# Kernel tuning notes

Measured on AMD Instinct MI355X. Metric: run time of the kernel, lower is better.

The kernel has to match this reference:

```python
import jax, jax.numpy as jnp
import numpy as np

N_ELEC = 64
IN_C = 64
HID = [64, 128]
OUT_C = 128
BATCH = 2048
BN_EPS = 1e-5


def build_graph():
    """Replicates EEGGraphNet._build_graph_structure with random 3D electrode positions."""
    rng = np.random.RandomState(0)
    pos = rng.rand(N_ELEC, 3).astype(np.float64)
    d = np.sqrt(((pos[:, None, :] - pos[None, :, :]) ** 2).sum(-1))
    thr = np.percentile(d[d > 0], 30)
    src, dst = [], []
    for i in range(N_ELEC):
        for j in range(i + 1, N_ELEC):
            if d[i, j] < thr:
                src += [i, j]
                dst += [j, i]
    return np.asarray(src, np.int32), np.asarray(dst, np.int32)


def setup_inputs() -> dict:
    key = jax.random.key(0)
    ks = jax.random.split(key, 8)
    src, dst = build_graph()
    dims = [IN_C] + HID + [OUT_C]  # [64, 64, 128, 128]
    inp = {"x": jax.random.normal(ks[0], (BATCH, N_ELEC, IN_C), jnp.float32)}
    for li in range(3):
        fi, fo = dims[li], dims[li + 1]
        inp[f"W{li+1}"] = jax.random.normal(ks[li + 1], (fi, fo), jnp.float32) * (1.0 / np.sqrt(fi))
        inp[f"b{li+1}"] = jnp.zeros((fo,), jnp.float32)
    for li in range(2):  # BN after first two convs
        inp[f"g{li+1}"] = jnp.ones((dims[li + 1],), jnp.float32)
        inp[f"be{li+1}"] = jnp.zeros((dims[li + 1],), jnp.float32)
    inp["src"] = jnp.asarray(src)
    inp["dst"] = jnp.asarray(dst)
    return inp


def gcn_conv(x, W, b, src, dst, edge_norm, self_norm):
    # x: (B, N, Fin) -> (B, N, Fout). GCN with self-loops, symmetric norm.
    h = jnp.einsum("bnf,fo->bno", x, W)
    msg = h[:, src, :] * edge_norm[None, :, None]          # (B, E, Fout) gather
    agg = jnp.zeros_like(h).at[:, dst, :].add(msg)         # scatter-add over dst
    return agg + h * self_norm[None, :, None] + b


def batchnorm(x, g, be):
    # torch BatchNorm1d over flattened (B*N, C) nodes, training-mode batch stats
    m = jnp.mean(x, axis=(0, 1))
    v = jnp.mean((x - m) ** 2, axis=(0, 1))
    return g * (x - m) * jax.lax.rsqrt(v + BN_EPS) + be


def reference(x, W1, b1, W2, b2, W3, b3, g1, be1, g2, be2, src, dst):
    # degree (with self-loop) is identical across graphs in the batch
    deg = jnp.zeros((N_ELEC,), x.dtype).at[dst].add(1.0) + 1.0
    inv_sqrt = jax.lax.rsqrt(deg)
    edge_norm = inv_sqrt[src] * inv_sqrt[dst]
    self_norm = 1.0 / deg

    h = gcn_conv(x, W1, b1, src, dst, edge_norm, self_norm)
    h = jax.nn.relu(batchnorm(h, g1, be1))
    h = gcn_conv(h, W2, b2, src, dst, edge_norm, self_norm)
    h = jax.nn.relu(batchnorm(h, g2, be2))
    h = gcn_conv(h, W3, b3, src, dst, edge_norm, self_norm)
    return jnp.mean(h, axis=1)  # global mean pool over electrodes -> (B, OUT_C)
```

## Files before the change

kernel.cpp:

```cpp
#include <hip/hip_runtime.h>
#include <hip/hip_bf16.h>

typedef unsigned short ushortT;
typedef unsigned int uintT;
typedef __attribute__((ext_vector_type(8))) short short8;
typedef __attribute__((ext_vector_type(4))) float f32x4;

#define BATCH   2048
#define NELEC   64
#define BN_EPS  1e-5f

#define OFF_AMEAN  4096
#define OFF_SS1    4160
#define OFF_SS2    4288
#define OFF_PS1    4544
#define OFF_PQ1    8640
#define OFF_PS2    12736
#define OFF_PQ2    20928
#define OFF_ABF    29120
#define OFF_W1T    33216
#define OFF_W2T    37312
#define OFF_H1     45504
#define OFF_H2     4239808

#define MFMA(a, b, c) __builtin_amdgcn_mfma_f32_16x16x32_bf16(a, b, c, 0, 0, 0)

__device__ inline float bf2f(ushortT u) { return __uint_as_float(((uintT)u) << 16); }
__device__ inline ushortT f2bf(float f) {
  uintT u = __float_as_uint(f);
  u = (u + 0x7FFFu + ((u >> 16) & 1u)) >> 16;
  return (ushortT)u;
}
__device__ inline void split2(float f, ushortT& hi, ushortT& lo) {
  hi = f2bf(f);
  lo = f2bf(f - bf2f(hi));
}
__device__ inline void split8(const float* f, short8& hi, short8& lo) {
  #pragma unroll
  for (int e = 0; e < 8; ++e) {
    ushortT h, l;
    split2(f[e], h, l);
    hi[e] = (short)h; lo[e] = (short)l;
  }
}

__global__ __launch_bounds__(256) void prep_kernel(const int* __restrict__ src,
    const int* __restrict__ dst, int E,
    const float* __restrict__ W1, const float* __restrict__ W2,
    float* __restrict__ ws) {
  __shared__ float degS[NELEC];
  __shared__ float As[NELEC * NELEC];
  int t = threadIdx.x;
  if (t < NELEC) degS[t] = 1.0f;
  for (int i = t; i < NELEC * NELEC; i += 256) As[i] = 0.0f;
  __syncthreads();
  for (int e = t; e < E; e += 256) atomicAdd(&degS[dst[e]], 1.0f);
  __syncthreads();
  for (int e = t; e < E; e += 256) {
    float en = rsqrtf(degS[src[e]]) * rsqrtf(degS[dst[e]]);
    atomicAdd(&As[dst[e] * NELEC + src[e]], en);
  }
  __syncthreads();
  if (t < NELEC) As[t * NELEC + t] += 1.0f / degS[t];
  __syncthreads();
  ushortT* abf = (ushortT*)(ws + OFF_ABF);
  for (int i = t; i < 4096; i += 256) {
    ushortT hi, lo; split2(As[i], hi, lo);
    abf[i] = hi; abf[4096 + i] = lo;
  }
  if (t < NELEC) {
    float s = 0.0f;
    for (int n = 0; n < NELEC; ++n) s += As[n * NELEC + t];
    ws[OFF_AMEAN + t] = s * (1.0f / NELEC);
  }
  ushortT* w1t = (ushortT*)(ws + OFF_W1T);
  for (int i = t; i < 4096; i += 256) {
    int o = i >> 6, k = i & 63;
    ushortT hi, lo; split2(W1[k * 64 + o], hi, lo);
    w1t[i] = hi; w1t[4096 + i] = lo;
  }
  ushortT* w2t = (ushortT*)(ws + OFF_W2T);
  for (int i = t; i < 8192; i += 256) {
    int o = i >> 6, k = i & 63;
    ushortT hi, lo; split2(W2[k * 128 + o], hi, lo);
    w2t[i] = hi; w2t[8192 + i] = lo;
  }
}

__global__ __launch_bounds__(256) void layer1_mfma(const float* __restrict__ x,
    const float* __restrict__ b1, float* __restrict__ ws) {
  __shared__ ushortT TsH[4][16 * 72];
  __shared__ ushortT TsL[4][16 * 72];
  const int w = threadIdx.x >> 6, lane = threadIdx.x & 63;
  const int item = blockIdx.x * 4 + w;
  const int c = lane & 15, g = lane >> 4;
  const ushortT* abf = (const ushortT*)(ws + OFF_ABF);
  const ushortT* w1t = (const ushortT*)(ws + OFF_W1T);
  ushortT* h1p = (ushortT*)(ws + OFF_H1) + (size_t)item * 4096;
  ushortT* tsh = &TsH[w][0];
  ushortT* tsl = &TsL[w][0];

  short8 Xhi[4][2], Xlo[4][2];
  #pragma unroll
  for (int rt = 0; rt < 4; ++rt) {
    #pragma unroll
    for (int ks = 0; ks < 2; ++ks) {
      const float* p = x + (size_t)item * 4096 + (rt * 16 + c) * 64 + ks * 32 + g * 8;
      float4 fa = *(const float4*)p;
      float4 fb = *(const float4*)(p + 4);
      float f[8] = {fa.x, fa.y, fa.z, fa.w, fb.x, fb.y, fb.z, fb.w};
      split8(f, Xhi[rt][ks], Xlo[rt][ks]);
    }
  }

  for (int s = 0; s < 4; ++s) {
    f32x4 t[4] = {{0,0,0,0},{0,0,0,0},{0,0,0,0},{0,0,0,0}};
    #pragma unroll
    for (int ks = 0; ks < 2; ++ks) {
      short8 bh = *(const short8*)(w1t + (s * 16 + c) * 64 + ks * 32 + g * 8);
      short8 bl = *(const short8*)(w1t + 4096 + (s * 16 + c) * 64 + ks * 32 + g * 8);
      #pragma unroll
      for (int rt = 0; rt < 4; ++rt) {
        t[rt] = MFMA(Xhi[rt][ks], bh, t[rt]);
        t[rt] = MFMA(Xhi[rt][ks], bl, t[rt]);
        t[rt] = MFMA(Xlo[rt][ks], bh, t[rt]);
      }
    }
    #pragma unroll
    for (int rt = 0; rt < 4; ++rt) {
      ushortT h0, h1_, h2_, h3, l0, l1, l2, l3;
      split2(t[rt][0], h0, l0); split2(t[rt][1], h1_, l1);
      split2(t[rt][2], h2_, l2); split2(t[rt][3], h3, l3);
      uint2 wh, wl;
      wh.x = (uintT)h0 | ((uintT)h1_ << 16); wh.y = (uintT)h2_ | ((uintT)h3 << 16);
      wl.x = (uintT)l0 | ((uintT)l1 << 16);  wl.y = (uintT)l2 | ((uintT)l3 << 16);
      int idx = c * 72 + rt * 16 + g * 4;
      *(uint2*)(tsh + idx) = wh;
      *(uint2*)(tsl + idx) = wl;
    }
    f32x4 hacc[4] = {{0,0,0,0},{0,0,0,0},{0,0,0,0},{0,0,0,0}};
    #pragma unroll
    for (int ks = 0; ks < 2; ++ks) {
      short8 th = *(const short8*)(tsh + c * 72 + ks * 32 + g * 8);
      short8 tl = *(const short8*)(tsl + c * 72 + ks * 32 + g * 8);
      #pragma unroll
      for (int rt = 0; rt < 4; ++rt) {
        short8 ah = *(const short8*)(abf + (rt * 16 + c) * 64 + ks * 32 + g * 8);
        short8 al = *(const short8*)(abf + 4096 + (rt * 16 + c) * 64 + ks * 32 + g * 8);
        hacc[rt] = MFMA(ah, th, hacc[rt]);
        hacc[rt] = MFMA(ah, tl, hacc[rt]);
        hacc[rt] = MFMA(al, th, hacc[rt]);
      }
    }
    float bias = b1[s * 16 + c];
    float S = 0.0f, Q = 0.0f;
    #pragma unroll
    for (int rt = 0; rt < 4; ++rt) {
      #pragma unroll
      for (int r = 0; r < 4; ++r) {
        float v = hacc[rt][r] + bias;
        S += v; Q += v * v;
        h1p[(rt * 16 + g * 4 + r) * 64 + s * 16 + c] = f2bf(v);
      }
    }
    S += __shfl_xor(S, 16); S += __shfl_xor(S, 32);
    Q += __shfl_xor(Q, 16); Q += __shfl_xor(Q, 32);
    if (g == 0) {
      int slot = item & 63;
      atomicAdd(&ws[OFF_PS1 + slot * 64 + s * 16 + c], S);
      atomicAdd(&ws[OFF_PQ1 + slot * 64 + s * 16 + c], Q);
    }
  }
}

__global__ void reduce1_kernel(const float* __restrict__ g1, const float* __restrict__ be1,
                               float* __restrict__ ws) {
  int t = threadIdx.x;
  if (t < 64) {
    float S = 0.0f, Q = 0.0f;
    for (int s = 0; s < 64; ++s) { S += ws[OFF_PS1 + s * 64 + t]; Q += ws[OFF_PQ1 + s * 64 + t]; }
    const float inv = 1.0f / (float)(BATCH * NELEC);
    float m = S * inv;
    float v = fmaxf(Q * inv - m * m, 0.0f);
    float sc = g1[t] * rsqrtf(v + BN_EPS);
    ws[OFF_SS1 + t] = sc;
    ws[OFF_SS1 + 64 + t] = fmaf(-m, sc, be1[t]);
  }
}

__global__ void reduce2_kernel(const float* __restrict__ g2, const float* __restrict__ be2,
                               float* __restrict__ ws) {
  int t = threadIdx.x;
  if (t < 128) {
    float S = 0.0f, Q = 0.0f;
    for (int s = 0; s < 64; ++s) { S += ws[OFF_PS2 + s * 128 + t]; Q += ws[OFF_PQ2 + s * 128 + t]; }
    const float inv = 1.0f / (float)(BATCH * NELEC);
    float m = S * inv;
    float v = fmaxf(Q * inv - m * m, 0.0f);
    float sc = g2[t] * rsqrtf(v + BN_EPS);
    ws[OFF_SS2 + t] = sc;
    ws[OFF_SS2 + 128 + t] = fmaf(-m, sc, be2[t]);
  }
}

__global__ __launch_bounds__(256) void layer2_mfma(const float* __restrict__ b2,
    float* __restrict__ ws) {
  __shared__ ushortT TsH[4][16 * 72];
  __shared__ ushortT TsL[4][16 * 72];
  const int w = threadIdx.x >> 6, lane = threadIdx.x & 63;
  const int item = blockIdx.x * 4 + w;
  const int c = lane & 15, g = lane >> 4;
  const ushortT* abf = (const ushortT*)(ws + OFF_ABF);
  const ushortT* w2t = (const ushortT*)(ws + OFF_W2T);
  const ushortT* h1p = (const ushortT*)(ws + OFF_H1) + (size_t)item * 4096;
  ushortT* h2p = (ushortT*)(ws + OFF_H2) + (size_t)item * 8192;
  ushortT* tsh = &TsH[w][0];
  ushortT* tsl = &TsL[w][0];

  short8 Yhi[4][2], Ylo[4][2];
  #pragma unroll
  for (int ks = 0; ks < 2; ++ks) {
    const float* sp = ws + OFF_SS1 + ks * 32 + g * 8;
    const float* tp = ws + OFF_SS1 + 64 + ks * 32 + g * 8;
    float4 sa = *(const float4*)sp, sb = *(const float4*)(sp + 4);
    float4 ta = *(const float4*)tp, tb = *(const float4*)(tp + 4);
    float s8[8] = {sa.x, sa.y, sa.z, sa.w, sb.x, sb.y, sb.z, sb.w};
    float t8[8] = {ta.x, ta.y, ta.z, ta.w, tb.x, tb.y, tb.z, tb.w};
    #pragma unroll
    for (int rt = 0; rt < 4; ++rt) {
      short8 hv = *(const short8*)(h1p + (rt * 16 + c) * 64 + ks * 32 + g * 8);
      float f[8];
      #pragma unroll
      for (int e = 0; e < 8; ++e)
        f[e] = fmaxf(fmaf(bf2f((ushortT)hv[e]), s8[e], t8[e]), 0.0f);
      split8(f, Yhi[rt][ks], Ylo[rt][ks]);
    }
  }

  for (int s = 0; s < 8; ++s) {
    f32x4 t[4] = {{0,0,0,0},{0,0,0,0},{0,0,0,0},{0,0,0,0}};
    #pragma unroll
    for (int ks = 0; ks < 2; ++ks) {
      short8 bh = *(const short8*)(w2t + (s * 16 + c) * 64 + ks * 32 + g * 8);
      short8 bl = *(const short8*)(w2t + 8192 + (s * 16 + c) * 64 + ks * 32 + g * 8);
      #pragma unroll
      for (int rt = 0; rt < 4; ++rt) {
        t[rt] = MFMA(Yhi[rt][ks], bh, t[rt]);
        t[rt] = MFMA(Yhi[rt][ks], bl, t[rt]);
        t[rt] = MFMA(Ylo[rt][ks], bh, t[rt]);
      }
    }
    #pragma unroll
    for (int rt = 0; rt < 4; ++rt) {
      ushortT h0, h1_, h2_, h3, l0, l1, l2, l3;
      split2(t[rt][0], h0, l0); split2(t[rt][1], h1_, l1);
      split2(t[rt][2], h2_, l2); split2(t[rt][3], h3, l3);
      uint2 wh, wl;
      wh.x = (uintT)h0 | ((uintT)h1_ << 16); wh.y = (uintT)h2_ | ((uintT)h3 << 16);
      wl.x = (uintT)l0 | ((uintT)l1 << 16);  wl.y = (uintT)l2 | ((uintT)l3 << 16);
      int idx = c * 72 + rt * 16 + g * 4;
      *(uint2*)(tsh + idx) = wh;
      *(uint2*)(tsl + idx) = wl;
    }
    f32x4 hacc[4] = {{0,0,0,0},{0,0,0,0},{0,0,0,0},{0,0,0,0}};
    #pragma unroll
    for (int ks = 0; ks < 2; ++ks) {
      short8 th = *(const short8*)(tsh + c * 72 + ks * 32 + g * 8);
      short8 tl = *(const short8*)(tsl + c * 72 + ks * 32 + g * 8);
      #pragma unroll
      for (int rt = 0; rt < 4; ++rt) {
        short8 ah = *(const short8*)(abf + (rt * 16 + c) * 64 + ks * 32 + g * 8);
        short8 al = *(const short8*)(abf + 4096 + (rt * 16 + c) * 64 + ks * 32 + g * 8);
        hacc[rt] = MFMA(ah, th, hacc[rt]);
        hacc[rt] = MFMA(ah, tl, hacc[rt]);
        hacc[rt] = MFMA(al, th, hacc[rt]);
      }
    }
    float bias = b2[s * 16 + c];
    float S = 0.0f, Q = 0.0f;
    #pragma unroll
    for (int rt = 0; rt < 4; ++rt) {
      #pragma unroll
      for (int r = 0; r < 4; ++r) {
        float v = hacc[rt][r] + bias;
        S += v; Q += v * v;
        h2p[(rt * 16 + g * 4 + r) * 128 + s * 16 + c] = f2bf(v);
      }
    }
    S += __shfl_xor(S, 16); S += __shfl_xor(S, 32);
    Q += __shfl_xor(Q, 16); Q += __shfl_xor(Q, 32);
    if (g == 0) {
      int slot = item & 63;
      atomicAdd(&ws[OFF_PS2 + slot * 128 + s * 16 + c], S);
      atomicAdd(&ws[OFF_PQ2 + slot * 128 + s * 16 + c], Q);
    }
  }
}

__global__ __launch_bounds__(256) void layer3_kernel(const float* __restrict__ W3,
    const float* __restrict__ b3, const float* __restrict__ ws,
    float* __restrict__ out) {
  const int w = threadIdx.x >> 6, lane = threadIdx.x & 63;
  const int item = blockIdx.x * 4 + w;
  const int f0 = lane * 2;
  const float s2a = ws[OFF_SS2 + f0],       s2b = ws[OFF_SS2 + f0 + 1];
  const float t2a = ws[OFF_SS2 + 128 + f0], t2b = ws[OFF_SS2 + 128 + f0 + 1];
  const float* am = ws + OFF_AMEAN;
  const ushortT* h2 = (const ushortT*)(ws + OFF_H2) + (size_t)item * 8192;
  float v0 = 0.0f, v1 = 0.0f;
  #pragma unroll 8
  for (int m = 0; m < 64; ++m) {
    uintT pk = *(const uintT*)(h2 + m * 128 + f0);
    float y0 = fmaxf(fmaf(bf2f((ushortT)(pk & 0xffffu)), s2a, t2a), 0.0f);
    float y1 = fmaxf(fmaf(bf2f((ushortT)(pk >> 16)),     s2b, t2b), 0.0f);
    float a = am[m];
    v0 = fmaf(a, y0, v0);
    v1 = fmaf(a, y1, v1);
  }
  float o0 = b3[f0], o1 = b3[f0 + 1];
  #pragma unroll 8
  for (int k = 0; k < 128; ++k) {
    float vk = __shfl((k & 1) ? v1 : v0, k >> 1, 64);
    o0 = fmaf(vk, W3[k * 128 + f0],     o0);
    o1 = fmaf(vk, W3[k * 128 + f0 + 1], o1);
  }
  float2 ov; ov.x = o0; ov.y = o1;
  *(float2*)(out + (size_t)item * 128 + f0) = ov;
}

extern "C" void kernel_launch(void* const* d_in, const int* in_sizes, int n_in,
                              void* d_out, int out_size, void* d_ws, size_t ws_size,
                              hipStream_t stream) {
  const float* x   = (const float*)d_in[0];
  const float* W1  = (const float*)d_in[1];
  const float* b1  = (const float*)d_in[2];
  const float* W2  = (const float*)d_in[3];
  const float* b2  = (const float*)d_in[4];
  const float* W3  = (const float*)d_in[5];
  const float* b3  = (const float*)d_in[6];
  const float* g1  = (const float*)d_in[7];
  const float* be1 = (const float*)d_in[8];
  const float* g2  = (const float*)d_in[9];
  const float* be2 = (const float*)d_in[10];
  const int*   src = (const int*)d_in[11];
  const int*   dst = (const int*)d_in[12];
  const int E = in_sizes[11];
  float* ws  = (float*)d_ws;
  float* out = (float*)d_out;

  hipMemsetAsync((void*)(ws + OFF_PS1), 0, (size_t)(29120 - OFF_PS1) * 4, stream);
  hipLaunchKernelGGL(prep_kernel,   dim3(1),   dim3(256), 0, stream, src, dst, E, W1, W2, ws);
  hipLaunchKernelGGL(layer1_mfma,   dim3(512), dim3(256), 0, stream, x, b1, ws);
  hipLaunchKernelGGL(reduce1_kernel,dim3(1),   dim3(64),  0, stream, g1, be1, ws);
  hipLaunchKernelGGL(layer2_mfma,   dim3(512), dim3(256), 0, stream, b2, ws);
  hipLaunchKernelGGL(reduce2_kernel,dim3(1),   dim3(128), 0, stream, g2, be2, ws);
  hipLaunchKernelGGL(layer3_kernel, dim3(512), dim3(256), 0, stream, W3, b3, ws, out);
}
```

Baseline: 200.9 us.

## Process one graph per block, split output column tiles across waves

Each layer kernel now gives one batch item to a whole 256-thread block, and the four waves split the output feature tiles instead of each wave looping over all tiles. Inputs are loaded coalesced into shared memory, split into hi/lo bf16 there and shared by all waves. Intermediate activations are stored tile-major (16-column blocks) so the per-wave writes are contiguous, and layer 3 reads with the matching layout. This raises parallelism and shortens the serial per-wave loop, at the cost of a block barrier and more shared memory per block.

```diff
diff --git a/kernel.cpp b/kernel.cpp
--- a/kernel.cpp
+++ b/kernel.cpp
@@ -87,89 +87,100 @@
   }
 }
 
-__global__ __launch_bounds__(256) void layer1_mfma(const float* __restrict__ x,
+__global__ __launch_bounds__(256, 4) void layer1_mfma(const float* __restrict__ x,
     const float* __restrict__ b1, float* __restrict__ ws) {
-  __shared__ ushortT TsH[4][16 * 72];
-  __shared__ ushortT TsL[4][16 * 72];
-  const int w = threadIdx.x >> 6, lane = threadIdx.x & 63;
-  const int item = blockIdx.x * 4 + w;
-  const int c = lane & 15, g = lane >> 4;
+  __shared__ ushortT FH[4096];
+  __shared__ ushortT FL[4096];
+  __shared__ ushortT Ts[4][2][1152];
+  const int item = blockIdx.x, t = threadIdx.x;
+  {
+    const int m = t >> 2, q = t & 3;
+    const float* xp = x + (size_t)item * 4096 + m * 64 + q * 16;
+    float f[16];
+    *(float4*)&f[0]  = *(const float4*)(xp);
+    *(float4*)&f[4]  = *(const float4*)(xp + 4);
+    *(float4*)&f[8]  = *(const float4*)(xp + 8);
+    *(float4*)&f[12] = *(const float4*)(xp + 12);
+    short8 h0, l0, h1v, l1v;
+    split8(f, h0, l0);
+    split8(f + 8, h1v, l1v);
+    const int base = q * 1024 + m * 8;
+    *(short8*)&FH[base] = h0; *(short8*)&FH[base + 512] = h1v;
+    *(short8*)&FL[base] = l0; *(short8*)&FL[base + 512] = l1v;
+  }
+  __syncthreads();
+  const int w = t >> 6, lane = t & 63, c = lane & 15, g = lane >> 4;
+  short8 Xhi[4][2], Xlo[4][2];
+  #pragma unroll
+  for (int rt = 0; rt < 4; ++rt) {
+    #pragma unroll
+    for (int ks = 0; ks < 2; ++ks) {
+      const int a = (ks * 4 + g) * 512 + (rt * 16 + c) * 8;
+      Xhi[rt][ks] = *(const short8*)&FH[a];
+      Xlo[rt][ks] = *(const short8*)&FL[a];
+    }
+  }
   const ushortT* abf = (const ushortT*)(ws + OFF_ABF);
   const ushortT* w1t = (const ushortT*)(ws + OFF_W1T);
-  ushortT* h1p = (ushortT*)(ws + OFF_H1) + (size_t)item * 4096;
-  ushortT* tsh = &TsH[w][0];
-  ushortT* tsl = &TsL[w][0];
-
-  short8 Xhi[4][2], Xlo[4][2];
+  ushortT* tsh = &Ts[w][0][0];
+  ushortT* tsl = &Ts[w][1][0];
+  const int s = w;
+  f32x4 tacc[4] = {{0,0,0,0},{0,0,0,0},{0,0,0,0},{0,0,0,0}};
+  #pragma unroll
+  for (int ks = 0; ks < 2; ++ks) {
+    short8 bh = *(const short8*)(w1t + (s * 16 + c) * 64 + ks * 32 + g * 8);
+    short8 bl = *(const short8*)(w1t + 4096 + (s * 16 + c) * 64 + ks * 32 + g * 8);
+    #pragma unroll
+    for (int rt = 0; rt < 4; ++rt) {
+      tacc[rt] = MFMA(Xhi[rt][ks], bh, tacc[rt]);
+      tacc[rt] = MFMA(Xhi[rt][ks], bl, tacc[rt]);
+      tacc[rt] = MFMA(Xlo[rt][ks], bh, tacc[rt]);
+    }
+  }
   #pragma unroll
   for (int rt = 0; rt < 4; ++rt) {
-    #pragma unroll
-    for (int ks = 0; ks < 2; ++ks) {
-      const float* p = x + (size_t)item * 4096 + (rt * 16 + c) * 64 + ks * 32 + g * 8;
-      float4 fa = *(const float4*)p;
-      float4 fb = *(const float4*)(p + 4);
-      float f[8] = {fa.x, fa.y, fa.z, fa.w, fb.x, fb.y, fb.z, fb.w};
-      split8(f, Xhi[rt][ks], Xlo[rt][ks]);
-    }
-  }
-
-  for (int s = 0; s < 4; ++s) {
-    f32x4 t[4] = {{0,0,0,0},{0,0,0,0},{0,0,0,0},{0,0,0,0}};
-    #pragma unroll
-    for (int ks = 0; ks < 2; ++ks) {
-      short8 bh = *(const short8*)(w1t + (s * 16 + c) * 64 + ks * 32 + g * 8);
-      short8 bl = *(const short8*)(w1t + 4096 + (s * 16 + c) * 64 + ks * 32 + g * 8);
-      #pragma unroll
-      for (int rt = 0; rt < 4; ++rt) {
-        t[rt] = MFMA(Xhi[rt][ks], bh, t[rt]);
-        t[rt] = MFMA(Xhi[rt][ks], bl, t[rt]);
-        t[rt] = MFMA(Xlo[rt][ks], bh, t[rt]);
-      }
-    }
+    ushortT h0, h1_, h2_, h3, l0, l1, l2, l3;
+    split2(tacc[rt][0], h0, l0); split2(tacc[rt][1], h1_, l1);
+    split2(tacc[rt][2], h2_, l2); split2(tacc[rt][3], h3, l3);
+    uint2 wh, wl;
+    wh.x = (uintT)h0 | ((uintT)h1_ << 16); wh.y = (uintT)h2_ | ((uintT)h3 << 16);
+    wl.x = (uintT)l0 | ((uintT)l1 << 16);  wl.y = (uintT)l2 | ((uintT)l3 << 16);
+    const int idx = c * 72 + rt * 16 + g * 4;
+    *(uint2*)(tsh + idx) = wh;
+    *(uint2*)(tsl + idx) = wl;
+  }
+  f32x4 hacc[4] = {{0,0,0,0},{0,0,0,0},{0,0,0,0},{0,0,0,0}};
+  #pragma unroll
+  for (int ks = 0; ks < 2; ++ks) {
+    short8 th = *(const short8*)(tsh + c * 72 + ks * 32 + g * 8);
+    short8 tl = *(const short8*)(tsl + c * 72 + ks * 32 + g * 8);
     #pragma unroll
     for (int rt = 0; rt < 4; ++rt) {
-      ushortT h0, h1_, h2_, h3, l0, l1, l2, l3;
-      split2(t[rt][0], h0, l0); split2(t[rt][1], h1_, l1);
-      split2(t[rt][2], h2_, l2); split2(t[rt][3], h3, l3);
-      uint2 wh, wl;
-      wh.x = (uintT)h0 | ((uintT)h1_ << 16); wh.y = (uintT)h2_ | ((uintT)h3 << 16);
-      wl.x = (uintT)l0 | ((uintT)l1 << 16);  wl.y = (uintT)l2 | ((uintT)l3 << 16);
-      int idx = c * 72 + rt * 16 + g * 4;
-      *(uint2*)(tsh + idx) = wh;
-      *(uint2*)(tsl + idx) = wl;
-    }
-    f32x4 hacc[4] = {{0,0,0,0},{0,0,0,0},{0,0,0,0},{0,0,0,0}};
-    #pragma unroll
-    for (int ks = 0; ks < 2; ++ks) {
-      short8 th = *(const short8*)(tsh + c * 72 + ks * 32 + g * 8);
-      short8 tl = *(const short8*)(tsl + c * 72 + ks * 32 + g * 8);
-      #pragma unroll
-      for (int rt = 0; rt < 4; ++rt) {
-        short8 ah = *(const short8*)(abf + (rt * 16 + c) * 64 + ks * 32 + g * 8);
-        short8 al = *(const short8*)(abf + 4096 + (rt * 16 + c) * 64 + ks * 32 + g * 8);
-        hacc[rt] = MFMA(ah, th, hacc[rt]);
-        hacc[rt] = MFMA(ah, tl, hacc[rt]);
-        hacc[rt] = MFMA(al, th, hacc[rt]);
-      }
-    }
-    float bias = b1[s * 16 + c];
-    float S = 0.0f, Q = 0.0f;
-    #pragma unroll
-    for (int rt = 0; rt < 4; ++rt) {
-      #pragma unroll
-      for (int r = 0; r < 4; ++r) {
-        float v = hacc[rt][r] + bias;
-        S += v; Q += v * v;
-        h1p[(rt * 16 + g * 4 + r) * 64 + s * 16 + c] = f2bf(v);
-      }
-    }
-    S += __shfl_xor(S, 16); S += __shfl_xor(S, 32);
-    Q += __shfl_xor(Q, 16); Q += __shfl_xor(Q, 32);
-    if (g == 0) {
-      int slot = item & 63;
-      atomicAdd(&ws[OFF_PS1 + slot * 64 + s * 16 + c], S);
-      atomicAdd(&ws[OFF_PQ1 + slot * 64 + s * 16 + c], Q);
-    }
+      short8 ah = *(const short8*)(abf + (rt * 16 + c) * 64 + ks * 32 + g * 8);
+      short8 al = *(const short8*)(abf + 4096 + (rt * 16 + c) * 64 + ks * 32 + g * 8);
+      hacc[rt] = MFMA(ah, th, hacc[rt]);
+      hacc[rt] = MFMA(ah, tl, hacc[rt]);
+      hacc[rt] = MFMA(al, th, hacc[rt]);
+    }
+  }
+  const float bias = b1[s * 16 + c];
+  ushortT* h1p = (ushortT*)(ws + OFF_H1) + (size_t)item * 4096 + s * 1024;
+  float S = 0.0f, Q = 0.0f;
+  #pragma unroll
+  for (int rt = 0; rt < 4; ++rt) {
+    #pragma unroll
+    for (int r = 0; r < 4; ++r) {
+      float v = hacc[rt][r] + bias;
+      S += v; Q += v * v;
+      h1p[(rt * 16 + g * 4 + r) * 16 + c] = f2bf(v);
+    }
+  }
+  S += __shfl_xor(S, 16); S += __shfl_xor(S, 32);
+  Q += __shfl_xor(Q, 16); Q += __shfl_xor(Q, 32);
+  if (g == 0) {
+    const int slot = item & 63;
+    atomicAdd(&ws[OFF_PS1 + slot * 64 + s * 16 + c], S);
+    atomicAdd(&ws[OFF_PQ1 + slot * 64 + s * 16 + c], Q);
   }
 }
 
@@ -203,62 +214,75 @@
   }
 }
 
-__global__ __launch_bounds__(256) void layer2_mfma(const float* __restrict__ b2,
+__global__ __launch_bounds__(256, 4) void layer2_mfma(const float* __restrict__ b2,
     float* __restrict__ ws) {
-  __shared__ ushortT TsH[4][16 * 72];
-  __shared__ ushortT TsL[4][16 * 72];
-  const int w = threadIdx.x >> 6, lane = threadIdx.x & 63;
-  const int item = blockIdx.x * 4 + w;
-  const int c = lane & 15, g = lane >> 4;
+  __shared__ ushortT FH[4096];
+  __shared__ ushortT FL[4096];
+  __shared__ ushortT Ts[4][2][1152];
+  const int item = blockIdx.x, t = threadIdx.x;
+  {
+    const int m = t >> 2, q = t & 3, k0 = q * 16;
+    const ushortT* hp = (const ushortT*)(ws + OFF_H1) + (size_t)item * 4096 + q * 1024 + m * 16;
+    short8 ha = *(const short8*)hp;
+    short8 hb = *(const short8*)(hp + 8);
+    const float* s1 = ws + OFF_SS1 + k0;
+    const float* t1 = ws + OFF_SS1 + 64 + k0;
+    float f[16];
+    #pragma unroll
+    for (int e = 0; e < 8; ++e)
+      f[e] = fmaxf(fmaf(bf2f((ushortT)ha[e]), s1[e], t1[e]), 0.0f);
+    #pragma unroll
+    for (int e = 0; e < 8; ++e)
+      f[8 + e] = fmaxf(fmaf(bf2f((ushortT)hb[e]), s1[8 + e], t1[8 + e]), 0.0f);
+    short8 h0, l0, h1v, l1v;
+    split8(f, h0, l0);
+    split8(f + 8, h1v, l1v);
+    const int base = q * 1024 + m * 8;
+    *(short8*)&FH[base] = h0; *(short8*)&FH[base + 512] = h1v;
+    *(short8*)&FL[base] = l0; *(short8*)&FL[base + 512] = l1v;
+  }
+  __syncthreads();
+  const int w = t >> 6, lane = t & 63, c = lane & 15, g = lane >> 4;
+  short8 Yhi[4][2], Ylo[4][2];
+  #pragma unroll
+  for (int rt = 0; rt < 4; ++rt) {
+    #pragma unroll
+    for (int ks = 0; ks < 2; ++ks) {
+      const int a = (ks * 4 + g) * 512 + (rt * 16 + c) * 8;
+      Yhi[rt][ks] = *(const short8*)&FH[a];
+      Ylo[rt][ks] = *(const short8*)&FL[a];
+    }
+  }
   const ushortT* abf = (const ushortT*)(ws + OFF_ABF);
   const ushortT* w2t = (const ushortT*)(ws + OFF_W2T);
-  const ushortT* h1p = (const ushortT*)(ws + OFF_H1) + (size_t)item * 4096;
-  ushortT* h2p = (ushortT*)(ws + OFF_H2) + (size_t)item * 8192;
-  ushortT* tsh = &TsH[w][0];
-  ushortT* tsl = &TsL[w][0];
-
-  short8 Yhi[4][2], Ylo[4][2];
-  #pragma unroll
-  for (int ks = 0; ks < 2; ++ks) {
-    const float* sp = ws + OFF_SS1 + ks * 32 + g * 8;
-    const float* tp = ws + OFF_SS1 + 64 + ks * 32 + g * 8;
-    float4 sa = *(const float4*)sp, sb = *(const float4*)(sp + 4);
-    float4 ta = *(const float4*)tp, tb = *(const float4*)(tp + 4);
-    float s8[8] = {sa.x, sa.y, sa.z, sa.w, sb.x, sb.y, sb.z, sb.w};
-    float t8[8] = {ta.x, ta.y, ta.z, ta.w, tb.x, tb.y, tb.z, tb.w};
-    #pragma unroll
-    for (int rt = 0; rt < 4; ++rt) {
-      short8 hv = *(const short8*)(h1p + (rt * 16 + c) * 64 + ks * 32 + g * 8);
-      float f[8];
-      #pragma unroll
-      for (int e = 0; e < 8; ++e)
-        f[e] = fmaxf(fmaf(bf2f((ushortT)hv[e]), s8[e], t8[e]), 0.0f);
-      split8(f, Yhi[rt][ks], Ylo[rt][ks]);
-    }
-  }
-
-  for (int s = 0; s < 8; ++s) {
-    f32x4 t[4] = {{0,0,0,0},{0,0,0,0},{0,0,0,0},{0,0,0,0}};
+  ushortT* tsh = &Ts[w][0][0];
+  ushortT* tsl = &Ts[w][1][0];
+  ushortT* h2p0 = (ushortT*)(ws + OFF_H2) + (size_t)item * 8192;
+
+  #pragma unroll
+  for (int si = 0; si < 2; ++si) {
+    const int s = w * 2 + si;
+    f32x4 tacc[4] = {{0,0,0,0},{0,0,0,0},{0,0,0,0},{0,0,0,0}};
     #pragma unroll
     for (int ks = 0; ks < 2; ++ks) {
       short8 bh = *(const short8*)(w2t + (s * 16 + c) * 64 + ks * 32 + g * 8);
       short8 bl = *(const short8*)(w2t + 8192 + (s * 16 + c) * 64 + ks * 32 + g * 8);
       #pragma unroll
       for (int rt = 0; rt < 4; ++rt) {
-        t[rt] = MFMA(Yhi[rt][ks], bh, t[rt]);
-        t[rt] = MFMA(Yhi[rt][ks], bl, t[rt]);
-        t[rt] = MFMA(Ylo[rt][ks], bh, t[rt]);
+        tacc[rt] = MFMA(Yhi[rt][ks], bh, tacc[rt]);
+        tacc[rt] = MFMA(Yhi[rt][ks], bl, tacc[rt]);
+        tacc[rt] = MFMA(Ylo[rt][ks], bh, tacc[rt]);
       }
     }
     #pragma unroll
     for (int rt = 0; rt < 4; ++rt) {
       ushortT h0, h1_, h2_, h3, l0, l1, l2, l3;
-      split2(t[rt][0], h0, l0); split2(t[rt][1], h1_, l1);
-      split2(t[rt][2], h2_, l2); split2(t[rt][3], h3, l3);
+      split2(tacc[rt][0], h0, l0); split2(tacc[rt][1], h1_, l1);
+      split2(tacc[rt][2], h2_, l2); split2(tacc[rt][3], h3, l3);
       uint2 wh, wl;
       wh.x = (uintT)h0 | ((uintT)h1_ << 16); wh.y = (uintT)h2_ | ((uintT)h3 << 16);
       wl.x = (uintT)l0 | ((uintT)l1 << 16);  wl.y = (uintT)l2 | ((uintT)l3 << 16);
-      int idx = c * 72 + rt * 16 + g * 4;
+      const int idx = c * 72 + rt * 16 + g * 4;
       *(uint2*)(tsh + idx) = wh;
       *(uint2*)(tsl + idx) = wl;
     }
@@ -276,7 +300,8 @@
         hacc[rt] = MFMA(al, th, hacc[rt]);
       }
     }
-    float bias = b2[s * 16 + c];
+    const float bias = b2[s * 16 + c];
+    ushortT* h2p = h2p0 + s * 1024;
     float S = 0.0f, Q = 0.0f;
     #pragma unroll
     for (int rt = 0; rt < 4; ++rt) {
@@ -284,33 +309,33 @@
       for (int r = 0; r < 4; ++r) {
         float v = hacc[rt][r] + bias;
         S += v; Q += v * v;
-        h2p[(rt * 16 + g * 4 + r) * 128 + s * 16 + c] = f2bf(v);
+        h2p[(rt * 16 + g * 4 + r) * 16 + c] = f2bf(v);
       }
     }
     S += __shfl_xor(S, 16); S += __shfl_xor(S, 32);
     Q += __shfl_xor(Q, 16); Q += __shfl_xor(Q, 32);
     if (g == 0) {
-      int slot = item & 63;
+      const int slot = item & 63;
       atomicAdd(&ws[OFF_PS2 + slot * 128 + s * 16 + c], S);
       atomicAdd(&ws[OFF_PQ2 + slot * 128 + s * 16 + c], Q);
     }
   }
 }
 
-__global__ __launch_bounds__(256) void layer3_kernel(const float* __restrict__ W3,
+__global__ __launch_bounds__(64) void layer3_kernel(const float* __restrict__ W3,
     const float* __restrict__ b3, const float* __restrict__ ws,
     float* __restrict__ out) {
-  const int w = threadIdx.x >> 6, lane = threadIdx.x & 63;
-  const int item = blockIdx.x * 4 + w;
+  const int item = blockIdx.x, lane = threadIdx.x;
   const int f0 = lane * 2;
   const float s2a = ws[OFF_SS2 + f0],       s2b = ws[OFF_SS2 + f0 + 1];
   const float t2a = ws[OFF_SS2 + 128 + f0], t2b = ws[OFF_SS2 + 128 + f0 + 1];
   const float* am = ws + OFF_AMEAN;
-  const ushortT* h2 = (const ushortT*)(ws + OFF_H2) + (size_t)item * 8192;
+  const ushortT* h2 = (const ushortT*)(ws + OFF_H2) + (size_t)item * 8192
+                      + (f0 >> 4) * 1024 + (f0 & 15);
   float v0 = 0.0f, v1 = 0.0f;
   #pragma unroll 8
   for (int m = 0; m < 64; ++m) {
-    uintT pk = *(const uintT*)(h2 + m * 128 + f0);
+    uintT pk = *(const uintT*)(h2 + m * 16);
     float y0 = fmaxf(fmaf(bf2f((ushortT)(pk & 0xffffu)), s2a, t2a), 0.0f);
     float y1 = fmaxf(fmaf(bf2f((ushortT)(pk >> 16)),     s2b, t2b), 0.0f);
     float a = am[m];
@@ -349,10 +374,10 @@
   float* out = (float*)d_out;
 
   hipMemsetAsync((void*)(ws + OFF_PS1), 0, (size_t)(29120 - OFF_PS1) * 4, stream);
-  hipLaunchKernelGGL(prep_kernel,   dim3(1),   dim3(256), 0, stream, src, dst, E, W1, W2, ws);
-  hipLaunchKernelGGL(layer1_mfma,   dim3(512), dim3(256), 0, stream, x, b1, ws);
-  hipLaunchKernelGGL(reduce1_kernel,dim3(1),   dim3(64),  0, stream, g1, be1, ws);
-  hipLaunchKernelGGL(layer2_mfma,   dim3(512), dim3(256), 0, stream, b2, ws);
-  hipLaunchKernelGGL(reduce2_kernel,dim3(1),   dim3(128), 0, stream, g2, be2, ws);
-  hipLaunchKernelGGL(layer3_kernel, dim3(512), dim3(256), 0, stream, W3, b3, ws, out);
-}
+  hipLaunchKernelGGL(prep_kernel,   dim3(1),     dim3(256), 0, stream, src, dst, E, W1, W2, ws);
+  hipLaunchKernelGGL(layer1_mfma,   dim3(BATCH), dim3(256), 0, stream, x, b1, ws);
+  hipLaunchKernelGGL(reduce1_kernel,dim3(1),     dim3(64),  0, stream, g1, be1, ws);
+  hipLaunchKernelGGL(layer2_mfma,   dim3(BATCH), dim3(256), 0, stream, b2, ws);
+  hipLaunchKernelGGL(reduce2_kernel,dim3(1),     dim3(128), 0, stream, g2, be2, ws);
+  hipLaunchKernelGGL(layer3_kernel, dim3(BATCH), dim3(64),  0, stream, W3, b3, ws, out);
+}
```

Measured after the change: 201.3 us. No clear change (+0.2%).

## Split fused per-layer GCN into separate weight-GEMM and adjacency-GEMM kernels

Applied to the files above, without the earlier changes.

Each GCN layer used to be one fused kernel that ran the X*W product, staged the split-precision result in shared memory, and then multiplied by the dense adjacency. It is now two kernels: one computes T=X*W and writes it transposed to global memory as a single bf16 term, and a second applies the adjacency with hi/lo adjacency fragments held in registers and reduces the BN statistics over shuffles. The bf16 split is also simplified to a truncating high part. The aim is to cut shared-memory staging and the third MFMA term on the adjacency product, at the cost of an extra global round-trip of the intermediate, two more launches, and lower precision of the intermediate.

```diff
diff --git a/kernel.cpp b/kernel.cpp
--- a/kernel.cpp
+++ b/kernel.cpp
@@ -21,7 +21,9 @@
 #define OFF_W1T    33216
 #define OFF_W2T    37312
 #define OFF_H1     45504
-#define OFF_H2     4239808
+#define OFF_T1     4239808
+#define OFF_T2     4239808
+#define OFF_H2     12628416
 
 #define MFMA(a, b, c) __builtin_amdgcn_mfma_f32_16x16x32_bf16(a, b, c, 0, 0, 0)
 
@@ -35,12 +37,13 @@
   hi = f2bf(f);
   lo = f2bf(f - bf2f(hi));
 }
-__device__ inline void split8(const float* f, short8& hi, short8& lo) {
+__device__ inline void splitT8(const float* f, short8& hi, short8& lo) {
   #pragma unroll
   for (int e = 0; e < 8; ++e) {
-    ushortT h, l;
-    split2(f[e], h, l);
-    hi[e] = (short)h; lo[e] = (short)l;
+    uintT u = __float_as_uint(f[e]);
+    float fh = __uint_as_float(u & 0xFFFF0000u);
+    hi[e] = (short)(u >> 16);
+    lo[e] = (short)f2bf(f[e] - fh);
   }
 }
 
@@ -87,88 +90,106 @@
   }
 }
 
-__global__ __launch_bounds__(256) void layer1_mfma(const float* __restrict__ x,
-    const float* __restrict__ b1, float* __restrict__ ws) {
-  __shared__ ushortT TsH[4][16 * 72];
-  __shared__ ushortT TsL[4][16 * 72];
-  const int w = threadIdx.x >> 6, lane = threadIdx.x & 63;
-  const int item = blockIdx.x * 4 + w;
+__global__ __launch_bounds__(256) void wgemm1_kernel(const float* __restrict__ x,
+    float* __restrict__ ws) {
+  const int t = threadIdx.x, w = t >> 6, lane = t & 63;
   const int c = lane & 15, g = lane >> 4;
-  const ushortT* abf = (const ushortT*)(ws + OFF_ABF);
+  const int b = blockIdx.x * 4 + w;
   const ushortT* w1t = (const ushortT*)(ws + OFF_W1T);
-  ushortT* h1p = (ushortT*)(ws + OFF_H1) + (size_t)item * 4096;
-  ushortT* tsh = &TsH[w][0];
-  ushortT* tsl = &TsL[w][0];
-
-  short8 Xhi[4][2], Xlo[4][2];
+  ushortT* t1 = (ushortT*)(ws + OFF_T1) + (size_t)b * 4096;
+
+  short8 Xh[4][2], Xl[4][2];
   #pragma unroll
   for (int rt = 0; rt < 4; ++rt) {
     #pragma unroll
     for (int ks = 0; ks < 2; ++ks) {
-      const float* p = x + (size_t)item * 4096 + (rt * 16 + c) * 64 + ks * 32 + g * 8;
-      float4 fa = *(const float4*)p;
-      float4 fb = *(const float4*)(p + 4);
+      const float* p = x + (size_t)b * 4096 + (rt * 16 + c) * 64 + ks * 32 + g * 8;
+      float4 fa = *(const float4*)p, fb = *(const float4*)(p + 4);
       float f[8] = {fa.x, fa.y, fa.z, fa.w, fb.x, fb.y, fb.z, fb.w};
-      split8(f, Xhi[rt][ks], Xlo[rt][ks]);
-    }
-  }
-
+      splitT8(f, Xh[rt][ks], Xl[rt][ks]);
+    }
+  }
+  #pragma unroll
   for (int s = 0; s < 4; ++s) {
-    f32x4 t[4] = {{0,0,0,0},{0,0,0,0},{0,0,0,0},{0,0,0,0}};
+    f32x4 acc[4] = {{0,0,0,0},{0,0,0,0},{0,0,0,0},{0,0,0,0}};
     #pragma unroll
     for (int ks = 0; ks < 2; ++ks) {
       short8 bh = *(const short8*)(w1t + (s * 16 + c) * 64 + ks * 32 + g * 8);
       short8 bl = *(const short8*)(w1t + 4096 + (s * 16 + c) * 64 + ks * 32 + g * 8);
       #pragma unroll
       for (int rt = 0; rt < 4; ++rt) {
-        t[rt] = MFMA(Xhi[rt][ks], bh, t[rt]);
-        t[rt] = MFMA(Xhi[rt][ks], bl, t[rt]);
-        t[rt] = MFMA(Xlo[rt][ks], bh, t[rt]);
+        acc[rt] = MFMA(Xh[rt][ks], bh, acc[rt]);
+        acc[rt] = MFMA(Xh[rt][ks], bl, acc[rt]);
+        acc[rt] = MFMA(Xl[rt][ks], bh, acc[rt]);
       }
     }
     #pragma unroll
     for (int rt = 0; rt < 4; ++rt) {
-      ushortT h0, h1_, h2_, h3, l0, l1, l2, l3;
-      split2(t[rt][0], h0, l0); split2(t[rt][1], h1_, l1);
-      split2(t[rt][2], h2_, l2); split2(t[rt][3], h3, l3);
-      uint2 wh, wl;
-      wh.x = (uintT)h0 | ((uintT)h1_ << 16); wh.y = (uintT)h2_ | ((uintT)h3 << 16);
-      wl.x = (uintT)l0 | ((uintT)l1 << 16);  wl.y = (uintT)l2 | ((uintT)l3 << 16);
-      int idx = c * 72 + rt * 16 + g * 4;
-      *(uint2*)(tsh + idx) = wh;
-      *(uint2*)(tsl + idx) = wl;
-    }
-    f32x4 hacc[4] = {{0,0,0,0},{0,0,0,0},{0,0,0,0},{0,0,0,0}};
-    #pragma unroll
-    for (int ks = 0; ks < 2; ++ks) {
-      short8 th = *(const short8*)(tsh + c * 72 + ks * 32 + g * 8);
-      short8 tl = *(const short8*)(tsl + c * 72 + ks * 32 + g * 8);
+      uint2 pk;
+      pk.x = (uintT)f2bf(acc[rt][0]) | ((uintT)f2bf(acc[rt][1]) << 16);
+      pk.y = (uintT)f2bf(acc[rt][2]) | ((uintT)f2bf(acc[rt][3]) << 16);
+      *(uint2*)(t1 + (s * 16 + c) * 64 + rt * 16 + 4 * g) = pk;
+    }
+  }
+}
+
+__global__ __launch_bounds__(256) void agemm1_kernel(const float* __restrict__ b1,
+    float* __restrict__ ws) {
+  const int t = threadIdx.x, w = t >> 6, lane = t & 63;
+  const int c = lane & 15, g = lane >> 4;
+  const int wg = blockIdx.x * 4 + w;
+  const int ns = wg & 3;
+  const int b0 = (wg >> 2) * 2;
+  const ushortT* abf = (const ushortT*)(ws + OFF_ABF);
+  short8 Bh[2], Bl[2];
+  #pragma unroll
+  for (int ks = 0; ks < 2; ++ks) {
+    Bh[ks] = *(const short8*)(abf + (ns * 16 + c) * 64 + ks * 32 + g * 8);
+    Bl[ks] = *(const short8*)(abf + 4096 + (ns * 16 + c) * 64 + ks * 32 + g * 8);
+  }
+  float Sa[4][4] = {}, Qa[4][4] = {};
+  #pragma unroll
+  for (int ib = 0; ib < 2; ++ib) {
+    const int b = b0 + ib;
+    const ushortT* t1 = (const ushortT*)(ws + OFF_T1) + (size_t)b * 4096;
+    ushortT* h1 = (ushortT*)(ws + OFF_H1) + (size_t)b * 4096;
+    #pragma unroll
+    for (int rt = 0; rt < 4; ++rt) {
+      f32x4 acc = {0, 0, 0, 0};
       #pragma unroll
-      for (int rt = 0; rt < 4; ++rt) {
-        short8 ah = *(const short8*)(abf + (rt * 16 + c) * 64 + ks * 32 + g * 8);
-        short8 al = *(const short8*)(abf + 4096 + (rt * 16 + c) * 64 + ks * 32 + g * 8);
-        hacc[rt] = MFMA(ah, th, hacc[rt]);
-        hacc[rt] = MFMA(ah, tl, hacc[rt]);
-        hacc[rt] = MFMA(al, th, hacc[rt]);
-      }
-    }
-    float bias = b1[s * 16 + c];
-    float S = 0.0f, Q = 0.0f;
-    #pragma unroll
-    for (int rt = 0; rt < 4; ++rt) {
-      #pragma unroll
-      for (int r = 0; r < 4; ++r) {
-        float v = hacc[rt][r] + bias;
-        S += v; Q += v * v;
-        h1p[(rt * 16 + g * 4 + r) * 64 + s * 16 + c] = f2bf(v);
-      }
-    }
-    S += __shfl_xor(S, 16); S += __shfl_xor(S, 32);
-    Q += __shfl_xor(Q, 16); Q += __shfl_xor(Q, 32);
-    if (g == 0) {
-      int slot = item & 63;
-      atomicAdd(&ws[OFF_PS1 + slot * 64 + s * 16 + c], S);
-      atomicAdd(&ws[OFF_PQ1 + slot * 64 + s * 16 + c], Q);
+      for (int ks = 0; ks < 2; ++ks) {
+        short8 tf = *(const short8*)(t1 + (rt * 16 + c) * 64 + ks * 32 + g * 8);
+        acc = MFMA(tf, Bh[ks], acc);
+        acc = MFMA(tf, Bl[ks], acc);
+      }
+      float4 bv = *(const float4*)(b1 + rt * 16 + 4 * g);
+      float v0 = acc[0] + bv.x, v1 = acc[1] + bv.y;
+      float v2 = acc[2] + bv.z, v3 = acc[3] + bv.w;
+      Sa[rt][0] += v0; Qa[rt][0] += v0 * v0;
+      Sa[rt][1] += v1; Qa[rt][1] += v1 * v1;
+      Sa[rt][2] += v2; Qa[rt][2] += v2 * v2;
+      Sa[rt][3] += v3; Qa[rt][3] += v3 * v3;
+      uint2 pk;
+      pk.x = (uintT)f2bf(v0) | ((uintT)f2bf(v1) << 16);
+      pk.y = (uintT)f2bf(v2) | ((uintT)f2bf(v3) << 16);
+      *(uint2*)(h1 + (ns * 16 + c) * 64 + rt * 16 + 4 * g) = pk;
+    }
+  }
+  const int slot = blockIdx.x & 63;
+  #pragma unroll
+  for (int rt = 0; rt < 4; ++rt) {
+    #pragma unroll
+    for (int r = 0; r < 4; ++r) {
+      float S = Sa[rt][r], Q = Qa[rt][r];
+      S += __shfl_xor(S, 1); S += __shfl_xor(S, 2);
+      S += __shfl_xor(S, 4); S += __shfl_xor(S, 8);
+      Q += __shfl_xor(Q, 1); Q += __shfl_xor(Q, 2);
+      Q += __shfl_xor(Q, 4); Q += __shfl_xor(Q, 8);
+      if (c == 0) {
+        const int ch = rt * 16 + 4 * g + r;
+        atomicAdd(&ws[OFF_PS1 + slot * 64 + ch], S);
+        atomicAdd(&ws[OFF_PQ1 + slot * 64 + ch], Q);
+      }
     }
   }
 }
@@ -203,96 +224,120 @@
   }
 }
 
-__global__ __launch_bounds__(256) void layer2_mfma(const float* __restrict__ b2,
-    float* __restrict__ ws) {
-  __shared__ ushortT TsH[4][16 * 72];
-  __shared__ ushortT TsL[4][16 * 72];
-  const int w = threadIdx.x >> 6, lane = threadIdx.x & 63;
-  const int item = blockIdx.x * 4 + w;
+__global__ __launch_bounds__(256) void wgemm2_kernel(float* __restrict__ ws) {
+  const int t = threadIdx.x, w = t >> 6, lane = t & 63;
   const int c = lane & 15, g = lane >> 4;
-  const ushortT* abf = (const ushortT*)(ws + OFF_ABF);
+  const int b = blockIdx.x * 4 + w;
   const ushortT* w2t = (const ushortT*)(ws + OFF_W2T);
-  const ushortT* h1p = (const ushortT*)(ws + OFF_H1) + (size_t)item * 4096;
-  ushortT* h2p = (ushortT*)(ws + OFF_H2) + (size_t)item * 8192;
-  ushortT* tsh = &TsH[w][0];
-  ushortT* tsl = &TsL[w][0];
-
-  short8 Yhi[4][2], Ylo[4][2];
+  const ushortT* h1 = (const ushortT*)(ws + OFF_H1) + (size_t)b * 4096;
+  ushortT* t2 = (ushortT*)(ws + OFF_T2) + (size_t)b * 8192;
+
+  float s1v[2][8], t1v[2][8];
   #pragma unroll
   for (int ks = 0; ks < 2; ++ks) {
     const float* sp = ws + OFF_SS1 + ks * 32 + g * 8;
     const float* tp = ws + OFF_SS1 + 64 + ks * 32 + g * 8;
     float4 sa = *(const float4*)sp, sb = *(const float4*)(sp + 4);
     float4 ta = *(const float4*)tp, tb = *(const float4*)(tp + 4);
-    float s8[8] = {sa.x, sa.y, sa.z, sa.w, sb.x, sb.y, sb.z, sb.w};
-    float t8[8] = {ta.x, ta.y, ta.z, ta.w, tb.x, tb.y, tb.z, tb.w};
-    #pragma unroll
-    for (int rt = 0; rt < 4; ++rt) {
-      short8 hv = *(const short8*)(h1p + (rt * 16 + c) * 64 + ks * 32 + g * 8);
+    s1v[ks][0]=sa.x; s1v[ks][1]=sa.y; s1v[ks][2]=sa.z; s1v[ks][3]=sa.w;
+    s1v[ks][4]=sb.x; s1v[ks][5]=sb.y; s1v[ks][6]=sb.z; s1v[ks][7]=sb.w;
+    t1v[ks][0]=ta.x; t1v[ks][1]=ta.y; t1v[ks][2]=ta.z; t1v[ks][3]=ta.w;
+    t1v[ks][4]=tb.x; t1v[ks][5]=tb.y; t1v[ks][6]=tb.z; t1v[ks][7]=tb.w;
+  }
+  short8 Yh[4][2], Yl[4][2];
+  #pragma unroll
+  for (int rt = 0; rt < 4; ++rt) {
+    #pragma unroll
+    for (int ks = 0; ks < 2; ++ks) {
+      short8 hv = *(const short8*)(h1 + (rt * 16 + c) * 64 + ks * 32 + g * 8);
       float f[8];
       #pragma unroll
       for (int e = 0; e < 8; ++e)
-        f[e] = fmaxf(fmaf(bf2f((ushortT)hv[e]), s8[e], t8[e]), 0.0f);
-      split8(f, Yhi[rt][ks], Ylo[rt][ks]);
-    }
-  }
-
+        f[e] = fmaxf(fmaf(bf2f((ushortT)hv[e]), s1v[ks][e], t1v[ks][e]), 0.0f);
+      splitT8(f, Yh[rt][ks], Yl[rt][ks]);
+    }
+  }
+  #pragma unroll
   for (int s = 0; s < 8; ++s) {
-    f32x4 t[4] = {{0,0,0,0},{0,0,0,0},{0,0,0,0},{0,0,0,0}};
+    f32x4 acc[4] = {{0,0,0,0},{0,0,0,0},{0,0,0,0},{0,0,0,0}};
     #pragma unroll
     for (int ks = 0; ks < 2; ++ks) {
       short8 bh = *(const short8*)(w2t + (s * 16 + c) * 64 + ks * 32 + g * 8);
       short8 bl = *(const short8*)(w2t + 8192 + (s * 16 + c) * 64 + ks * 32 + g * 8);
       #pragma unroll
       for (int rt = 0; rt < 4; ++rt) {
-        t[rt] = MFMA(Yhi[rt][ks], bh, t[rt]);
-        t[rt] = MFMA(Yhi[rt][ks], bl, t[rt]);
-        t[rt] = MFMA(Ylo[rt][ks], bh, t[rt]);
+        acc[rt] = MFMA(Yh[rt][ks], bh, acc[rt]);
+        acc[rt] = MFMA(Yh[rt][ks], bl, acc[rt]);
+        acc[rt] = MFMA(Yl[rt][ks], bh, acc[rt]);
       }
     }
     #pragma unroll
     for (int rt = 0; rt < 4; ++rt) {
-      ushortT h0, h1_, h2_, h3, l0, l1, l2, l3;
-      split2(t[rt][0], h0, l0); split2(t[rt][1], h1_, l1);
-      split2(t[rt][2], h2_, l2); split2(t[rt][3], h3, l3);
-      uint2 wh, wl;
-      wh.x = (uintT)h0 | ((uintT)h1_ << 16); wh.y = (uintT)h2_ | ((uintT)h3 << 16);
-      wl.x = (uintT)l0 | ((uintT)l1 << 16);  wl.y = (uintT)l2 | ((uintT)l3 << 16);
-      int idx = c * 72 + rt * 16 + g * 4;
-      *(uint2*)(tsh + idx) = wh;
-      *(uint2*)(tsl + idx) = wl;
-    }
-    f32x4 hacc[4] = {{0,0,0,0},{0,0,0,0},{0,0,0,0},{0,0,0,0}};
-    #pragma unroll
-    for (int ks = 0; ks < 2; ++ks) {
-      short8 th = *(const short8*)(tsh + c * 72 + ks * 32 + g * 8);
-      short8 tl = *(const short8*)(tsl + c * 72 + ks * 32 + g * 8);
+      uint2 pk;
+      pk.x = (uintT)f2bf(acc[rt][0]) | ((uintT)f2bf(acc[rt][1]) << 16);
+      pk.y = (uintT)f2bf(acc[rt][2]) | ((uintT)f2bf(acc[rt][3]) << 16);
+      *(uint2*)(t2 + (s * 16 + c) * 64 + rt * 16 + 4 * g) = pk;
+    }
+  }
+}
+
+__global__ __launch_bounds__(256) void agemm2_kernel(const float* __restrict__ b2,
+    float* __restrict__ ws) {
+  const int t = threadIdx.x, w = t >> 6, lane = t & 63;
+  const int c = lane & 15, g = lane >> 4;
+  const int wg = blockIdx.x * 4 + w;
+  const int ns = wg & 3;
+  const int b0 = (wg >> 2) * 2;
+  const ushortT* abf = (const ushortT*)(ws + OFF_ABF);
+  short8 Bh[2], Bl[2];
+  #pragma unroll
+  for (int ks = 0; ks < 2; ++ks) {
+    Bh[ks] = *(const short8*)(abf + (ns * 16 + c) * 64 + ks * 32 + g * 8);
+    Bl[ks] = *(const short8*)(abf + 4096 + (ns * 16 + c) * 64 + ks * 32 + g * 8);
+  }
+  float Sa[8][4] = {}, Qa[8][4] = {};
+  #pragma unroll
+  for (int ib = 0; ib < 2; ++ib) {
+    const int b = b0 + ib;
+    const ushortT* t2 = (const ushortT*)(ws + OFF_T2) + (size_t)b * 8192;
+    ushortT* h2 = (ushortT*)(ws + OFF_H2) + (size_t)b * 8192;
+    #pragma unroll
+    for (int rt = 0; rt < 8; ++rt) {
+      f32x4 acc = {0, 0, 0, 0};
       #pragma unroll
-      for (int rt = 0; rt < 4; ++rt) {
-        short8 ah = *(const short8*)(abf + (rt * 16 + c) * 64 + ks * 32 + g * 8);
-        short8 al = *(const short8*)(abf + 4096 + (rt * 16 + c) * 64 + ks * 32 + g * 8);
-        hacc[rt] = MFMA(ah, th, hacc[rt]);
-        hacc[rt] = MFMA(ah, tl, hacc[rt]);
-        hacc[rt] = MFMA(al, th, hacc[rt]);
-      }
-    }
-    float bias = b2[s * 16 + c];
-    float S = 0.0f, Q = 0.0f;
-    #pragma unroll
-    for (int rt = 0; rt < 4; ++rt) {
-      #pragma unroll
-      for (int r = 0; r < 4; ++r) {
-        float v = hacc[rt][r] + bias;
-        S += v; Q += v * v;
-        h2p[(rt * 16 + g * 4 + r) * 128 + s * 16 + c] = f2bf(v);
-      }
-    }
-    S += __shfl_xor(S, 16); S += __shfl_xor(S, 32);
-    Q += __shfl_xor(Q, 16); Q += __shfl_xor(Q, 32);
-    if (g == 0) {
-      int slot = item & 63;
-      atomicAdd(&ws[OFF_PS2 + slot * 128 + s * 16 + c], S);
-      atomicAdd(&ws[OFF_PQ2 + slot * 128 + s * 16 + c], Q);
+      for (int ks = 0; ks < 2; ++ks) {
+        short8 tf = *(const short8*)(t2 + (rt * 16 + c) * 64 + ks * 32 + g * 8);
+        acc = MFMA(tf, Bh[ks], acc);
+        acc = MFMA(tf, Bl[ks], acc);
+      }
+      float4 bv = *(const float4*)(b2 + rt * 16 + 4 * g);
+      float v0 = acc[0] + bv.x, v1 = acc[1] + bv.y;
+      float v2 = acc[2] + bv.z, v3 = acc[3] + bv.w;
+      Sa[rt][0] += v0; Qa[rt][0] += v0 * v0;
+      Sa[rt][1] += v1; Qa[rt][1] += v1 * v1;
+      Sa[rt][2] += v2; Qa[rt][2] += v2 * v2;
+      Sa[rt][3] += v3; Qa[rt][3] += v3 * v3;
+      uint2 pk;
+      pk.x = (uintT)f2bf(v0) | ((uintT)f2bf(v1) << 16);
+      pk.y = (uintT)f2bf(v2) | ((uintT)f2bf(v3) << 16);
+      *(uint2*)(h2 + (ns * 16 + c) * 128 + rt * 16 + 4 * g) = pk;
+    }
+  }
+  const int slot = blockIdx.x & 63;
+  #pragma unroll
+  for (int rt = 0; rt < 8; ++rt) {
+    #pragma unroll
+    for (int r = 0; r < 4; ++r) {
+      float S = Sa[rt][r], Q = Qa[rt][r];
+      S += __shfl_xor(S, 1); S += __shfl_xor(S, 2);
+      S += __shfl_xor(S, 4); S += __shfl_xor(S, 8);
+      Q += __shfl_xor(Q, 1); Q += __shfl_xor(Q, 2);
+      Q += __shfl_xor(Q, 4); Q += __shfl_xor(Q, 8);
+      if (c == 0) {
+        const int ch = rt * 16 + 4 * g + r;
+        atomicAdd(&ws[OFF_PS2 + slot * 128 + ch], S);
+        atomicAdd(&ws[OFF_PQ2 + slot * 128 + ch], Q);
+      }
     }
   }
 }
@@ -349,10 +394,12 @@
   float* out = (float*)d_out;
 
   hipMemsetAsync((void*)(ws + OFF_PS1), 0, (size_t)(29120 - OFF_PS1) * 4, stream);
-  hipLaunchKernelGGL(prep_kernel,   dim3(1),   dim3(256), 0, stream, src, dst, E, W1, W2, ws);
-  hipLaunchKernelGGL(layer1_mfma,   dim3(512), dim3(256), 0, stream, x, b1, ws);
-  hipLaunchKernelGGL(reduce1_kernel,dim3(1),   dim3(64),  0, stream, g1, be1, ws);
-  hipLaunchKernelGGL(layer2_mfma,   dim3(512), dim3(256), 0, stream, b2, ws);
-  hipLaunchKernelGGL(reduce2_kernel,dim3(1),   dim3(128), 0, stream, g2, be2, ws);
-  hipLaunchKernelGGL(layer3_kernel, dim3(512), dim3(256), 0, stream, W3, b3, ws, out);
-}
+  hipLaunchKernelGGL(prep_kernel,   dim3(1),    dim3(256), 0, stream, src, dst, E, W1, W2, ws);
+  hipLaunchKernelGGL(wgemm1_kernel, dim3(512),  dim3(256), 0, stream, x, ws);
+  hipLaunchKernelGGL(agemm1_kernel, dim3(1024), dim3(256), 0, stream, b1, ws);
+  hipLaunchKernelGGL(reduce1_kernel,dim3(1),    dim3(64),  0, stream, g1, be1, ws);
+  hipLaunchKernelGGL(wgemm2_kernel, dim3(512),  dim3(256), 0, stream, ws);
+  hipLaunchKernelGGL(agemm2_kernel, dim3(1024), dim3(256), 0, stream, b2, ws);
+  hipLaunchKernelGGL(reduce2_kernel,dim3(1),    dim3(128), 0, stream, g2, be2, ws);
+  hipLaunchKernelGGL(layer3_kernel, dim3(512),  dim3(256), 0, stream, W3, b3, ws, out);
+}
```

Measured after the change: 225.0 us. +12.0%, slower.
